# Optimization experiments

Hardware: AMD Instinct MI355X
Metric: run time of the kernel (lower is better)

The kernel has to match this reference:

```python
import jax, jax.numpy as jnp
import numpy as np

N = 100000          # nodes
DEG = 32            # fixed in-degree (every node has a non-empty mailbox)
E = N * DEG         # edges
IN_DIM = 25         # node feature dim; 3 aggregators * 1 scaler * 25 = 75
OUT_DIM = 128
AGG_EPS = 1e-5      # PNA std aggregator epsilon
BN_EPS = 1e-5       # BatchNorm1d epsilon


def setup_inputs() -> dict:
    key = jax.random.key(0)
    k = jax.random.split(key, 6)
    h = jax.random.normal(k[0], (N, IN_DIM), dtype=jnp.float32)
    snorm_n = jax.random.uniform(k[1], (N, 1), dtype=jnp.float32)
    # every node appears exactly DEG times as a destination -> degree 32
    edge_dst = jnp.repeat(jnp.arange(N, dtype=jnp.int32), DEG)
    edge_src = jax.random.randint(k[2], (E,), 0, N, dtype=jnp.int32)
    # posttrans MLP (1 layer): Linear(75 -> 128), no final activation
    W = jax.random.normal(k[3], (3 * IN_DIM, OUT_DIM), dtype=jnp.float32) / np.sqrt(3 * IN_DIM)
    b = jnp.zeros((OUT_DIM,), dtype=jnp.float32)
    # BatchNorm1d affine params
    gamma = jnp.ones((OUT_DIM,), dtype=jnp.float32)
    beta = jnp.zeros((OUT_DIM,), dtype=jnp.float32)
    return {"h": h, "snorm_n": snorm_n, "edge_src": edge_src, "edge_dst": edge_dst,
            "W": W, "b": b, "gamma": gamma, "beta": beta}


def reference(h, snorm_n, edge_src, edge_dst, W, b, gamma, beta):
    # --- message: e = src node features (pretrans_edges + message_func) ---
    e = h[edge_src]                                   # [E, IN_DIM] irregular gather
    # --- reduce: mean / max / std over each destination's mailbox ---
    ones = jnp.ones((e.shape[0],), dtype=h.dtype)
    deg = jax.ops.segment_sum(ones, edge_dst, num_segments=N)
    deg = jnp.maximum(deg, 1.0)[:, None]              # [N, 1]
    s1 = jax.ops.segment_sum(e, edge_dst, num_segments=N)
    mean = s1 / deg                                   # aggregate_mean
    mx = jax.ops.segment_max(e, edge_dst, num_segments=N)  # aggregate_max
    s2 = jax.ops.segment_sum(e * e, edge_dst, num_segments=N)
    var = jax.nn.relu(s2 / deg - mean * mean)         # aggregate_var
    std = jnp.sqrt(var + AGG_EPS)                     # aggregate_std
    agg = jnp.concatenate([mean, mx, std], axis=1)    # [N, 75]; identity scaler only
    # --- posttrans MLP: single Linear(75 -> 128), last_activation='none' ---
    z = agg @ W + b                                   # [N, OUT_DIM]
    # --- graph norm ---
    z = z * snorm_n
    # --- BatchNorm1d (training mode: batch statistics, biased variance) ---
    mu = jnp.mean(z, axis=0)
    v = jnp.var(z, axis=0)
    z = (z - mu) / jnp.sqrt(v + BN_EPS) * gamma + beta
    # --- relu; residual disabled (in_dim != out_dim); dropout p=0.0 is no-op ---
    return jax.nn.relu(z)
```

## Files before the change

kernel.cpp:

```cpp
#include <hip/hip_runtime.h>

#define NN 100000
#define DEG 32
#define IN_DIM 25
#define AGG_DIM 75
#define OUT_DIM 128
#define NPB 10
#define NCHUNK (NN / NPB)
#define BLK 256

__global__ void zero_bn(float* bnbuf) {
    bnbuf[threadIdx.x] = 0.0f;
}

__global__ __launch_bounds__(BLK) void pna_main(
    const float* __restrict__ h, const float* __restrict__ snorm,
    const int* __restrict__ esrc, const float* __restrict__ W,
    const float* __restrict__ b, float* __restrict__ z,
    float* __restrict__ bnbuf)
{
    __shared__ int   eids[NPB * DEG];
    __shared__ float agg[NPB][AGG_DIM];
    __shared__ float red[2 * BLK];

    const int t = threadIdx.x;
    const int col  = t & 127;
    const int half = t >> 7;

    float wreg[AGG_DIM];
    #pragma unroll
    for (int k = 0; k < AGG_DIM; ++k) wreg[k] = W[k * OUT_DIM + col];
    const float bcol = b[col];

    const int nl_a = t / IN_DIM;
    const int f    = t - nl_a * IN_DIM;

    float bns = 0.0f, bnq = 0.0f;

    for (int chunk = blockIdx.x; chunk < NCHUNK; chunk += gridDim.x) {
        const int n0 = chunk * NPB;
        __syncthreads();
        for (int i = t; i < NPB * DEG; i += BLK) eids[i] = esrc[n0 * DEG + i];
        __syncthreads();

        if (t < NPB * IN_DIM) {
            float s = 0.f, q = 0.f, m = -3.4e38f;
            #pragma unroll
            for (int e = 0; e < DEG; ++e) {
                const int src = eids[nl_a * DEG + e];
                const float v = h[src * IN_DIM + f];
                s += v; q += v * v; m = fmaxf(m, v);
            }
            const float mean = s * (1.0f / DEG);
            const float var  = fmaxf(q * (1.0f / DEG) - mean * mean, 0.0f);
            agg[nl_a][f]              = mean;
            agg[nl_a][IN_DIM + f]     = m;
            agg[nl_a][2 * IN_DIM + f] = sqrtf(var + 1e-5f);
        }
        __syncthreads();

        #pragma unroll
        for (int p = 0; p < NPB / 2; ++p) {
            const int nl   = p * 2 + half;
            const int node = n0 + nl;
            float acc = bcol;
            #pragma unroll
            for (int k = 0; k < AGG_DIM; ++k) acc = fmaf(agg[nl][k], wreg[k], acc);
            acc *= snorm[node];
            z[node * OUT_DIM + col] = acc;
            bns += acc; bnq += acc * acc;
        }
    }

    __syncthreads();
    red[t] = bns; red[BLK + t] = bnq;
    __syncthreads();
    if (t < OUT_DIM) {
        atomicAdd(&bnbuf[t],           red[t]       + red[t + 128]);
        atomicAdd(&bnbuf[OUT_DIM + t], red[BLK + t] + red[BLK + t + 128]);
    }
}

__global__ __launch_bounds__(BLK) void bn_apply(
    const float* __restrict__ bnbuf, const float* __restrict__ gamma,
    const float* __restrict__ beta, float* __restrict__ z)
{
    __shared__ float sc_s[OUT_DIM], sh_s[OUT_DIM];
    const int t = threadIdx.x;
    if (t < OUT_DIM) {
        const float mu = bnbuf[t] * (1.0f / NN);
        const float v  = fmaxf(bnbuf[OUT_DIM + t] * (1.0f / NN) - mu * mu, 0.0f);
        const float sc = gamma[t] * rsqrtf(v + 1e-5f);
        sc_s[t] = sc;
        sh_s[t] = beta[t] - mu * sc;
    }
    __syncthreads();
    const int c4 = (t & 31) * 4;
    const float s0 = sc_s[c4], s1 = sc_s[c4+1], s2 = sc_s[c4+2], s3 = sc_s[c4+3];
    const float h0 = sh_s[c4], h1 = sh_s[c4+1], h2 = sh_s[c4+2], h3 = sh_s[c4+3];

    float4* z4 = (float4*)z;
    const int total4 = NN * (OUT_DIM / 4);
    for (int i = blockIdx.x * BLK + t; i < total4; i += gridDim.x * BLK) {
        float4 v = z4[i];
        v.x = fmaxf(fmaf(v.x, s0, h0), 0.f);
        v.y = fmaxf(fmaf(v.y, s1, h1), 0.f);
        v.z = fmaxf(fmaf(v.z, s2, h2), 0.f);
        v.w = fmaxf(fmaf(v.w, s3, h3), 0.f);
        z4[i] = v;
    }
}

extern "C" void kernel_launch(void* const* d_in, const int* in_sizes, int n_in,
                              void* d_out, int out_size, void* d_ws, size_t ws_size,
                              hipStream_t stream) {
    const float* h     = (const float*)d_in[0];
    const float* snorm = (const float*)d_in[1];
    const int*   esrc  = (const int*)d_in[2];
    const float* W     = (const float*)d_in[4];
    const float* b     = (const float*)d_in[5];
    const float* gamma = (const float*)d_in[6];
    const float* beta  = (const float*)d_in[7];
    float* z     = (float*)d_out;
    float* bnbuf = (float*)d_ws;

    zero_bn<<<1, 256, 0, stream>>>(bnbuf);
    pna_main<<<2048, BLK, 0, stream>>>(h, snorm, esrc, W, b, z, bnbuf);
    bn_apply<<<2048, BLK, 0, stream>>>(bnbuf, gamma, beta, z);
}
```

Measured before the change: 207.9 us.

## Gather bf16 node features and compute posttrans linear with MFMA

A prep kernel converts h to bf16 in workspace so the irregular gather moves half the bytes, and it also zeroes the BN buffer. The 75x128 linear is done with bf16 MFMA 16x16x32 on a padded shared agg tile instead of scalar FMAs from a register-held W column. Edge ids are read directly as int4 vectors instead of being staged through shared memory, and the BN partial sums are reduced with wave shuffles. This trades accuracy, from bf16 features, aggregates and weights, for less memory traffic and less compute, and it adds a full conversion pass over h.

```diff
diff --git a/kernel.cpp b/kernel.cpp
--- a/kernel.cpp
+++ b/kernel.cpp
@@ -1,83 +1,143 @@
 #include <hip/hip_runtime.h>
+#include <hip/hip_bf16.h>
 
 #define NN 100000
 #define DEG 32
 #define IN_DIM 25
 #define AGG_DIM 75
+#define KPAD 104
 #define OUT_DIM 128
 #define NPB 10
 #define NCHUNK (NN / NPB)
 #define BLK 256
+#define GRID 2048
 
-__global__ void zero_bn(float* bnbuf) {
-    bnbuf[threadIdx.x] = 0.0f;
+typedef __attribute__((ext_vector_type(8))) short short8;
+typedef __attribute__((ext_vector_type(4))) float f32x4;
+
+static __device__ __forceinline__ ushort f2bf(float x) {
+    __hip_bfloat16 h = __float2bfloat16(x);
+    return *reinterpret_cast<ushort*>(&h);
+}
+static __device__ __forceinline__ float bf2f(ushort u) {
+    return __uint_as_float(((unsigned)u) << 16);
+}
+
+__global__ __launch_bounds__(BLK) void prep(const float4* __restrict__ h4,
+                                            ushort4* __restrict__ hb4,
+                                            float* __restrict__ bnbuf) {
+    int i = blockIdx.x * BLK + threadIdx.x;
+    if (i < 2 * OUT_DIM) bnbuf[i] = 0.0f;
+    const int total = NN * IN_DIM / 4;
+    for (; i < total; i += GRID * BLK) {
+        float4 v = h4[i];
+        ushort4 o;
+        o.x = f2bf(v.x); o.y = f2bf(v.y); o.z = f2bf(v.z); o.w = f2bf(v.w);
+        hb4[i] = o;
+    }
 }
 
 __global__ __launch_bounds__(BLK) void pna_main(
-    const float* __restrict__ h, const float* __restrict__ snorm,
+    const ushort* __restrict__ hb, const float* __restrict__ snorm,
     const int* __restrict__ esrc, const float* __restrict__ W,
     const float* __restrict__ b, float* __restrict__ z,
     float* __restrict__ bnbuf)
 {
-    __shared__ int   eids[NPB * DEG];
-    __shared__ float agg[NPB][AGG_DIM];
-    __shared__ float red[2 * BLK];
+    __shared__ ushort agg[16][KPAD];
 
     const int t = threadIdx.x;
-    const int col  = t & 127;
-    const int half = t >> 7;
+    const int lane = t & 63;
+    const int wv = t >> 6;
 
-    float wreg[AGG_DIM];
+    for (int i = t; i < 16 * KPAD; i += BLK) ((ushort*)agg)[i] = 0;
+
+    const int cb0 = (wv * 2 + 0) * 16 + (lane & 15);
+    const int cb1 = (wv * 2 + 1) * 16 + (lane & 15);
+    short8 bfrag[2][3];
     #pragma unroll
-    for (int k = 0; k < AGG_DIM; ++k) wreg[k] = W[k * OUT_DIM + col];
-    const float bcol = b[col];
+    for (int ct = 0; ct < 2; ++ct) {
+        const int cb = ct ? cb1 : cb0;
+        #pragma unroll
+        for (int kt = 0; kt < 3; ++kt) {
+            short8 fr;
+            #pragma unroll
+            for (int j = 0; j < 8; ++j) {
+                const int k = kt * 32 + ((lane >> 4) * 8) + j;
+                const float w = (k < AGG_DIM) ? W[k * OUT_DIM + cb] : 0.0f;
+                fr[j] = (short)f2bf(w);
+            }
+            bfrag[ct][kt] = fr;
+        }
+    }
+    const float bb0 = b[cb0], bb1 = b[cb1];
 
-    const int nl_a = t / IN_DIM;
-    const int f    = t - nl_a * IN_DIM;
+    const int nl = t / IN_DIM;
+    const int f  = t - nl * IN_DIM;
+    const bool aggthread = (t < NPB * IN_DIM);
 
-    float bns = 0.0f, bnq = 0.0f;
+    float bns0 = 0.f, bnq0 = 0.f, bns1 = 0.f, bnq1 = 0.f;
 
-    for (int chunk = blockIdx.x; chunk < NCHUNK; chunk += gridDim.x) {
+    for (int chunk = blockIdx.x; chunk < NCHUNK; chunk += GRID) {
         const int n0 = chunk * NPB;
         __syncthreads();
-        for (int i = t; i < NPB * DEG; i += BLK) eids[i] = esrc[n0 * DEG + i];
-        __syncthreads();
-
-        if (t < NPB * IN_DIM) {
+        if (aggthread) {
+            const int4* e4 = reinterpret_cast<const int4*>(esrc + (n0 + nl) * DEG);
             float s = 0.f, q = 0.f, m = -3.4e38f;
             #pragma unroll
-            for (int e = 0; e < DEG; ++e) {
-                const int src = eids[nl_a * DEG + e];
-                const float v = h[src * IN_DIM + f];
-                s += v; q += v * v; m = fmaxf(m, v);
+            for (int eo = 0; eo < DEG / 4; ++eo) {
+                const int4 ee = e4[eo];
+                float v0 = bf2f(hb[ee.x * IN_DIM + f]);
+                float v1 = bf2f(hb[ee.y * IN_DIM + f]);
+                float v2 = bf2f(hb[ee.z * IN_DIM + f]);
+                float v3 = bf2f(hb[ee.w * IN_DIM + f]);
+                s += v0 + v1 + v2 + v3;
+                q = fmaf(v0, v0, q); q = fmaf(v1, v1, q);
+                q = fmaf(v2, v2, q); q = fmaf(v3, v3, q);
+                m = fmaxf(m, fmaxf(fmaxf(v0, v1), fmaxf(v2, v3)));
             }
             const float mean = s * (1.0f / DEG);
             const float var  = fmaxf(q * (1.0f / DEG) - mean * mean, 0.0f);
-            agg[nl_a][f]              = mean;
-            agg[nl_a][IN_DIM + f]     = m;
-            agg[nl_a][2 * IN_DIM + f] = sqrtf(var + 1e-5f);
+            agg[nl][f]              = f2bf(mean);
+            agg[nl][IN_DIM + f]     = f2bf(m);
+            agg[nl][2 * IN_DIM + f] = f2bf(sqrtf(var + 1e-5f));
         }
         __syncthreads();
 
+        const int arow = lane & 15;
+        const int ak0  = (lane >> 4) * 8;
+        f32x4 acc0 = {0.f, 0.f, 0.f, 0.f}, acc1 = {0.f, 0.f, 0.f, 0.f};
         #pragma unroll
-        for (int p = 0; p < NPB / 2; ++p) {
-            const int nl   = p * 2 + half;
-            const int node = n0 + nl;
-            float acc = bcol;
-            #pragma unroll
-            for (int k = 0; k < AGG_DIM; ++k) acc = fmaf(agg[nl][k], wreg[k], acc);
-            acc *= snorm[node];
-            z[node * OUT_DIM + col] = acc;
-            bns += acc; bnq += acc * acc;
+        for (int kt = 0; kt < 3; ++kt) {
+            const short8 afrag = *reinterpret_cast<const short8*>(&agg[arow][kt * 32 + ak0]);
+            acc0 = __builtin_amdgcn_mfma_f32_16x16x32_bf16(afrag, bfrag[0][kt], acc0, 0, 0, 0);
+            acc1 = __builtin_amdgcn_mfma_f32_16x16x32_bf16(afrag, bfrag[1][kt], acc1, 0, 0, 0);
+        }
+        const int r0 = (lane >> 4) * 4;
+        #pragma unroll
+        for (int r = 0; r < 4; ++r) {
+            const int row = r0 + r;
+            if (row < NPB) {
+                const int node = n0 + row;
+                const float sn = snorm[node];
+                const float v0 = (acc0[r] + bb0) * sn;
+                const float v1 = (acc1[r] + bb1) * sn;
+                z[node * OUT_DIM + cb0] = v0;
+                z[node * OUT_DIM + cb1] = v1;
+                bns0 += v0; bnq0 = fmaf(v0, v0, bnq0);
+                bns1 += v1; bnq1 = fmaf(v1, v1, bnq1);
+            }
         }
     }
 
-    __syncthreads();
-    red[t] = bns; red[BLK + t] = bnq;
-    __syncthreads();
-    if (t < OUT_DIM) {
-        atomicAdd(&bnbuf[t],           red[t]       + red[t + 128]);
-        atomicAdd(&bnbuf[OUT_DIM + t], red[BLK + t] + red[BLK + t + 128]);
+    bns0 += __shfl_xor(bns0, 16); bnq0 += __shfl_xor(bnq0, 16);
+    bns0 += __shfl_xor(bns0, 32); bnq0 += __shfl_xor(bnq0, 32);
+    bns1 += __shfl_xor(bns1, 16); bnq1 += __shfl_xor(bnq1, 16);
+    bns1 += __shfl_xor(bns1, 32); bnq1 += __shfl_xor(bnq1, 32);
+    if ((lane >> 4) == 0) {
+        atomicAdd(&bnbuf[cb0], bns0);
+        atomicAdd(&bnbuf[OUT_DIM + cb0], bnq0);
+        atomicAdd(&bnbuf[cb1], bns1);
+        atomicAdd(&bnbuf[OUT_DIM + cb1], bnq1);
     }
 }
 
@@ -121,10 +181,11 @@
     const float* b     = (const float*)d_in[5];
     const float* gamma = (const float*)d_in[6];
     const float* beta  = (const float*)d_in[7];
-    float* z     = (float*)d_out;
-    float* bnbuf = (float*)d_ws;
+    float*  z     = (float*)d_out;
+    float*  bnbuf = (float*)d_ws;
+    ushort* hb    = (ushort*)((char*)d_ws + 1024);
 
-    zero_bn<<<1, 256, 0, stream>>>(bnbuf);
-    pna_main<<<2048, BLK, 0, stream>>>(h, snorm, esrc, W, b, z, bnbuf);
-    bn_apply<<<2048, BLK, 0, stream>>>(bnbuf, gamma, beta, z);
+    prep<<<GRID, BLK, 0, stream>>>((const float4*)h, (ushort4*)hb, bnbuf);
+    pna_main<<<GRID, BLK, 0, stream>>>(hb, snorm, esrc, W, b, z, bnbuf);
+    bn_apply<<<GRID, BLK, 0, stream>>>(bnbuf, gamma, beta, z);
 }
```

After: 192.4 us. -7.5%, faster.
